# Kernel tuning notes

Measured on AMD Instinct MI355X. Metric: run time of the kernel, lower is better.

## Reference

```python
import jax, jax.numpy as jnp
import numpy as np

B, L, D1, D2 = 4, 2048, 1024, 1024

def setup_inputs() -> dict:
    key = jax.random.key(0)
    k1, k2, k3, k4, k5, k6 = jax.random.split(key, 6)
    s1 = 1.0 / np.sqrt(D1)
    s2 = 1.0 / np.sqrt(D2)
    return {
        "features_1": jax.random.normal(k1, (B, L, D1), dtype=jnp.float32),
        "features_2": jax.random.normal(k2, (B, L, D2), dtype=jnp.float32),
        # nn.Linear(d1, d2): W1 [d2, d1], b1 [d2]
        "W1": jax.random.uniform(k3, (D2, D1), jnp.float32, -s1, s1),
        "b1": jax.random.uniform(k4, (D2,), jnp.float32, -s1, s1),
        # nn.Linear(d2, d1): W2 [d1, d2], b2 [d1]
        "W2": jax.random.uniform(k5, (D1, D2), jnp.float32, -s2, s2),
        "b2": jax.random.uniform(k6, (D1,), jnp.float32, -s2, s2),
    }

def reference(features_1, features_2, W1, b1, W2, b2):
    # transformed_features_1: [B, L, D2]
    t1 = jnp.einsum('bld,ed->ble', features_1, W1) + b1
    # unscaled similarity: [B, L, L]
    sim = jnp.einsum('ble,bme->blm', t1, features_2)
    attn = jax.nn.softmax(sim, axis=-1)  # both softmaxes are identical
    attended_1 = jnp.einsum('blm,bme->ble', attn, features_2)  # [B, L, D2]
    attended_2 = jnp.einsum('blm,bme->ble', attn, t1)          # [B, L, D2]
    attended_2 = jnp.einsum('ble,de->bld', attended_2, W2) + b2  # [B, L, D1]
    return attended_1, attended_2
```

## Files before the change

kernel.cpp:

```cpp
#include <hip/hip_runtime.h>
#include <stdint.h>

#define BB 4
#define LL 2048
#define DD 1024

typedef __attribute__((ext_vector_type(4))) float f32x4;
typedef __attribute__((ext_vector_type(8))) _Float16 f16x8;
typedef __attribute__((ext_vector_type(4))) unsigned short u16x4;
typedef __attribute__((ext_vector_type(8))) unsigned short u16x8;
typedef unsigned short u16;

__device__ __forceinline__ u16 f2h(float x){
  return __builtin_bit_cast(u16, (_Float16)x);
}

__device__ __forceinline__ void gload16(const u16* g, u16* l){
  __builtin_amdgcn_global_load_lds((const __attribute__((address_space(1))) unsigned*)g,
                                   (__attribute__((address_space(3))) unsigned*)l,
                                   16, 0, 0);
}

__device__ __forceinline__ int xcd_swz(int bx, int nwg){
  return (bx & 7) * (nwg >> 3) + (bx >> 3);
}

__device__ __forceinline__ void stage_tile8(u16* lds, const u16* src, int ld, int wave, int lane){
  const int r0 = lane >> 3;
  const int cs = (((lane & 7) ^ r0) << 3);
  #pragma unroll
  for (int j = 0; j < 2; ++j){
    const int rb = wave*16 + j*8;
    gload16(src + (size_t)(rb + r0)*ld + cs, lds + rb*64);
  }
}

__device__ __forceinline__ f16x8 frag_ld(const u16* t, int row, int ko){
  return __builtin_bit_cast(f16x8,
    *reinterpret_cast<const f32x4*>(t + row*64 + (ko ^ ((row & 7) << 3))));
}

__global__ void cast3_k(const float* __restrict__ f1, u16* __restrict__ f1f,
                        const float* __restrict__ W1, u16* __restrict__ w1f,
                        const float* __restrict__ W2, u16* __restrict__ w2f){
  const int n1 = (BB*LL*DD)/4, nw = (DD*DD)/4;
  const int stride = gridDim.x * blockDim.x;
  for (int i = blockIdx.x*blockDim.x + threadIdx.x; i < n1 + 2*nw; i += stride){
    const float* s; u16* d; int k;
    if (i < n1){ s = f1; d = f1f; k = i; }
    else if (i < n1 + nw){ s = W1; d = w1f; k = i - n1; }
    else { s = W2; d = w2f; k = i - n1 - nw; }
    f32x4 v = reinterpret_cast<const f32x4*>(s)[k];
    u16x4 h;
    #pragma unroll
    for (int j = 0; j < 4; ++j) h[j] = f2h(v[j]);
    reinterpret_cast<u16x4*>(d)[k] = h;
  }
}

__global__ void castT_k(const float* __restrict__ f2, u16* __restrict__ f2f,
                        u16* __restrict__ f2T){
  __shared__ u16 t[32][33];
  const int b = blockIdx.z;
  const int d0 = blockIdx.x*32, l0 = blockIdx.y*32;
  const float* src = f2 + (size_t)b*LL*DD;
  u16* d1 = f2f + (size_t)b*LL*DD;
  u16* d2 = f2T + (size_t)b*DD*LL;
  const int x = threadIdx.x;
  for (int j = threadIdx.y; j < 32; j += 8){
    u16 h = f2h(src[(size_t)(l0+j)*DD + d0 + x]);
    d1[(size_t)(l0+j)*DD + d0 + x] = h;
    t[j][x] = h;
  }
  __syncthreads();
  for (int j = threadIdx.y; j < 32; j += 8)
    d2[(size_t)(d0+j)*LL + l0 + x] = t[x][j];
}

__global__ __launch_bounds__(512,2) void gemm8p_k(
    const u16* __restrict__ A_g, long long sAb, int lda,
    const u16* __restrict__ B_g, long long sBb, int ldb,
    float* __restrict__ C, long long sCb, int ldc, int NT){
  __shared__ __align__(16) u16 As[4][128*64];
  __shared__ __align__(16) u16 Bs[4][128*64];
  const int b = blockIdx.y;
  const int bx = xcd_swz(blockIdx.x, gridDim.x);
  const int bm = bx >> 3, bn = bx & 7;
  const int tid = threadIdx.x, wave = tid>>6, lane = tid&63;
  const int wm = wave & 1, wn = wave >> 1;
  const int r0 = lane >> 3, cs = (((lane&7) ^ r0) << 3);
  const int rb0 = wave*16;
  const u16* Ab = A_g + (size_t)b*sAb + (size_t)(bm*256)*lda;
  const u16* Bb = B_g + (size_t)b*sBb + (size_t)(bn*256)*ldb;

  f32x4 acc[2][2][4][2];
  #pragma unroll
  for (int i=0;i<2;i++)
    #pragma unroll
    for (int j=0;j<2;j++)
      #pragma unroll
      for (int m=0;m<4;m++)
        #pragma unroll
        for (int n=0;n<2;n++) acc[i][j][m][n] = (f32x4){0.f,0.f,0.f,0.f};

  auto stA = [&](int tt, int h){
    const u16* s = Ab + (size_t)(h*128 + rb0 + r0)*lda + (size_t)tt*64 + cs;
    u16* d = &As[((tt&1)<<1)+h][rb0*64];
    gload16(s, d);
    gload16(s + (size_t)8*lda, d + 8*64);
  };
  auto stB = [&](int tt, int h){
    const u16* s = Bb + (size_t)(h*128 + rb0 + r0)*ldb + (size_t)tt*64 + cs;
    u16* d = &Bs[((tt&1)<<1)+h][rb0*64];
    gload16(s, d);
    gload16(s + (size_t)8*ldb, d + 8*64);
  };

  stA(0,0); stB(0,0); stA(0,1); stB(0,1);
  stA(1,0); stB(1,0);
  asm volatile("s_waitcnt vmcnt(4)" ::: "memory");
  __builtin_amdgcn_s_barrier();

  for (int t = 0; t < NT; ++t){
    #pragma unroll
    for (int p = 0; p < 4; ++p){
      const u16* Ah = As[((t&1)<<1) + (p>>1)];
      const u16* Bh = Bs[((t&1)<<1) + (p&1)];
      f16x8 af[4][2], bf[2][2];
      #pragma unroll
      for (int mi=0;mi<4;mi++)
        #pragma unroll
        for (int ks=0;ks<2;ks++)
          af[mi][ks] = frag_ld(Ah, wm*64 + mi*16 + (lane&15), ks*32 + ((lane>>4)<<3));
      #pragma unroll
      for (int ni=0;ni<2;ni++)
        #pragma unroll
        for (int ks=0;ks<2;ks++)
          bf[ni][ks] = frag_ld(Bh, wn*32 + ni*16 + (lane&15), ks*32 + ((lane>>4)<<3));
      if (p == 0){ if (t+1 < NT) stA(t+1, 1); }
      else if (p == 1){ if (t+1 < NT) stB(t+1, 1); }
      else if (p == 2){ if (t+2 < NT) stA(t+2, 0); }
      else {
        if (t+2 < NT){ stB(t+2, 0); asm volatile("s_waitcnt vmcnt(4)" ::: "memory"); }
        else         {              asm volatile("s_waitcnt vmcnt(0)" ::: "memory"); }
      }
      __builtin_amdgcn_s_barrier();
      asm volatile("s_waitcnt lgkmcnt(0)" ::: "memory");
      __builtin_amdgcn_sched_barrier(0);
      __builtin_amdgcn_s_setprio(1);
      #pragma unroll
      for (int mi=0;mi<4;mi++)
        #pragma unroll
        for (int ni=0;ni<2;ni++)
          #pragma unroll
          for (int ks=0;ks<2;ks++)
            acc[p>>1][p&1][mi][ni] = __builtin_amdgcn_mfma_f32_16x16x32_f16(
                af[mi][ks], bf[ni][ks], acc[p>>1][p&1][mi][ni], 0,0,0);
      __builtin_amdgcn_s_setprio(0);
      __builtin_amdgcn_sched_barrier(0);
      __builtin_amdgcn_s_barrier();
    }
  }

  #pragma unroll
  for (int qm=0;qm<2;qm++)
    #pragma unroll
    for (int qn=0;qn<2;qn++)
      #pragma unroll
      for (int mi=0;mi<4;mi++)
        #pragma unroll
        for (int ni=0;ni<2;ni++){
          const int r = bm*256 + qm*128 + wm*64 + mi*16 + ((lane>>4)<<2);
          const int c = bn*256 + qn*128 + wn*32 + ni*16 + (lane&15);
          float* Cb = C + (size_t)b*sCb;
          #pragma unroll
          for (int j=0;j<4;j++)
            Cb[(size_t)(r+j)*ldc + c] = acc[qm][qn][mi][ni][j];
        }
}

__global__ __launch_bounds__(512,4) void gemm_t1_k(
    const u16* __restrict__ A_g, const u16* __restrict__ B_g,
    const float* __restrict__ bias, u16* __restrict__ Oh){
  __shared__ __align__(16) u16 As[128*64];
  __shared__ __align__(16) u16 Bs[128*64];
  const int bx = xcd_swz(blockIdx.x, gridDim.x);
  const int bm = bx >> 3, bn = bx & 7;
  const int tid = threadIdx.x, wave = tid>>6, lane = tid&63;
  const int wr = wave>>2, wc = wave&3;
  const u16* Ab = A_g + (size_t)(bm*128)*DD;
  const u16* Bb = B_g + (size_t)(bn*128)*DD;
  f32x4 acc[4][2];
  #pragma unroll
  for (int i=0;i<4;i++)
    #pragma unroll
    for (int j=0;j<2;j++) acc[i][j] = (f32x4){0.f,0.f,0.f,0.f};

  for (int k0 = 0; k0 < DD; k0 += 64){
    __syncthreads();
    stage_tile8(As, Ab + k0, DD, wave, lane);
    stage_tile8(Bs, Bb + k0, DD, wave, lane);
    __syncthreads();
    #pragma unroll
    for (int kk=0;kk<2;kk++){
      const int ko = kk*32 + ((lane>>4)<<3);
      f16x8 a[4], bb[2];
      #pragma unroll
      for (int mi=0;mi<4;mi++) a[mi]  = frag_ld(As, wr*64 + mi*16 + (lane&15), ko);
      #pragma unroll
      for (int ni=0;ni<2;ni++) bb[ni] = frag_ld(Bs, wc*32 + ni*16 + (lane&15), ko);
      #pragma unroll
      for (int mi=0;mi<4;mi++)
        #pragma unroll
        for (int ni=0;ni<2;ni++)
          acc[mi][ni] = __builtin_amdgcn_mfma_f32_16x16x32_f16(a[mi], bb[ni], acc[mi][ni], 0,0,0);
    }
  }
  #pragma unroll
  for (int mi=0;mi<4;mi++)
    #pragma unroll
    for (int ni=0;ni<2;ni++){
      const int r = bm*128 + wr*64 + mi*16 + ((lane>>4)<<2);
      const int c = bn*128 + wc*32 + ni*16 + (lane&15);
      const float bv = bias[c];
      #pragma unroll
      for (int j=0;j<4;j++)
        Oh[(size_t)(r+j)*DD + c] = f2h(acc[mi][ni][j] + bv);
    }
}

__global__ __launch_bounds__(256) void softmax_k(float* __restrict__ sim){
  const int row = blockIdx.x;
  float* p = sim + (size_t)row * LL;
  const int tid = threadIdx.x, wave = tid>>6, lane = tid&63;
  f32x4 x0 = reinterpret_cast<const f32x4*>(p)[tid];
  f32x4 x1 = reinterpret_cast<const f32x4*>(p)[tid + 256];
  float mx = fmaxf(fmaxf(fmaxf(x0[0],x0[1]), fmaxf(x0[2],x0[3])),
                   fmaxf(fmaxf(x1[0],x1[1]), fmaxf(x1[2],x1[3])));
  #pragma unroll
  for (int o = 32; o; o >>= 1) mx = fmaxf(mx, __shfl_xor(mx, o, 64));
  __shared__ float red[8];
  if (lane == 0) red[wave] = mx;
  __syncthreads();
  mx = fmaxf(fmaxf(red[0], red[1]), fmaxf(red[2], red[3]));
  float e0[4], e1[4], s = 0.f;
  #pragma unroll
  for (int j=0;j<4;j++){ e0[j] = __expf(x0[j]-mx); s += e0[j]; }
  #pragma unroll
  for (int j=0;j<4;j++){ e1[j] = __expf(x1[j]-mx); s += e1[j]; }
  #pragma unroll
  for (int o = 32; o; o >>= 1) s += __shfl_xor(s, o, 64);
  if (lane == 0) red[4+wave] = s;
  __syncthreads();
  s = (red[4]+red[5]) + (red[6]+red[7]);
  const float inv = 1.0f / s;
  u16* ob = reinterpret_cast<u16*>(p);
  u16x4 w0, w1;
  #pragma unroll
  for (int j=0;j<4;j++){ w0[j] = f2h(e0[j]*inv); w1[j] = f2h(e1[j]*inv); }
  reinterpret_cast<u16x4*>(ob)[tid]       = w0;
  reinterpret_cast<u16x4*>(ob)[tid + 256] = w1;
}

__global__ __launch_bounds__(512,4) void gemm_zt_k(const u16* __restrict__ t1f,
                                                   const u16* __restrict__ w2f,
                                                   u16* __restrict__ ZT){
  __shared__ __align__(16) u16 As[128*64];
  __shared__ __align__(16) u16 Bs[128*64];
  __shared__ u16 T[128*132];
  const int bx = xcd_swz(blockIdx.x, gridDim.x);
  const int bm = bx >> 3, bn = bx & 7;
  const int tid = threadIdx.x, wave = tid>>6, lane = tid&63;
  const int wr = wave>>2, wc = wave&3;
  const u16* Ab = t1f + (size_t)(bm*128)*DD;
  const u16* Bb = w2f + (size_t)(bn*128)*DD;
  f32x4 acc[4][2];
  #pragma unroll
  for (int i=0;i<4;i++)
    #pragma unroll
    for (int j=0;j<2;j++) acc[i][j] = (f32x4){0.f,0.f,0.f,0.f};

  for (int k0 = 0; k0 < DD; k0 += 64){
    __syncthreads();
    stage_tile8(As, Ab + k0, DD, wave, lane);
    stage_tile8(Bs, Bb + k0, DD, wave, lane);
    __syncthreads();
    #pragma unroll
    for (int kk=0;kk<2;kk++){
      const int ko = kk*32 + ((lane>>4)<<3);
      f16x8 a[4], bb[2];
      #pragma unroll
      for (int mi=0;mi<4;mi++) a[mi]  = frag_ld(As, wr*64 + mi*16 + (lane&15), ko);
      #pragma unroll
      for (int ni=0;ni<2;ni++) bb[ni] = frag_ld(Bs, wc*32 + ni*16 + (lane&15), ko);
      #pragma unroll
      for (int mi=0;mi<4;mi++)
        #pragma unroll
        for (int ni=0;ni<2;ni++)
          acc[mi][ni] = __builtin_amdgcn_mfma_f32_16x16x32_f16(a[mi], bb[ni], acc[mi][ni], 0,0,0);
    }
  }
  #pragma unroll
  for (int mi=0;mi<4;mi++)
    #pragma unroll
    for (int ni=0;ni<2;ni++){
      const int r = wr*64 + mi*16 + ((lane>>4)<<2);
      const int c = wc*32 + ni*16 + (lane&15);
      #pragma unroll
      for (int j=0;j<4;j++)
        T[(r+j)*132 + c] = f2h(acc[mi][ni][j]);
    }
  __syncthreads();
  const int b2i = bm >> 4;
  const int mb  = (bm*128) & 2047;
  const int d   = tid >> 2, m0 = (tid & 3) << 5;
  u16* dst = ZT + ((size_t)b2i*DD + bn*128 + d)*LL + mb + m0;
  #pragma unroll
  for (int g = 0; g < 4; ++g){
    u16x8 v;
    #pragma unroll
    for (int e = 0; e < 8; ++e) v[e] = T[(m0 + g*8 + e)*132 + d];
    *reinterpret_cast<u16x8*>(dst + g*8) = v;
  }
}

__global__ __launch_bounds__(512,4) void gemm_pv_k(const u16* __restrict__ attn,
                                                   const u16* __restrict__ f2T,
                                                   const u16* __restrict__ ZT,
                                                   float* __restrict__ out1,
                                                   float* __restrict__ out2,
                                                   const float* __restrict__ b2){
  __shared__ __align__(16) u16 As[128*64];
  __shared__ __align__(16) u16 Bs[128*64];
  const int b = blockIdx.y;
  const int bx = xcd_swz(blockIdx.x, gridDim.x);
  const int bm = bx >> 4, bn = bx & 15;
  const int tid = threadIdx.x, wave = tid>>6, lane = tid&63;
  const int wr = wave>>2, wc = wave&3;
  const u16* Ab = attn + (size_t)b*LL*4096 + (size_t)(bm*128)*4096;
  const u16* Bbase = (bn < 8) ? f2T : ZT;
  const int d0 = (bn & 7) * 128;
  const u16* Bb = Bbase + (size_t)b*DD*LL + (size_t)d0*LL;
  f32x4 acc[4][2];
  #pragma unroll
  for (int i=0;i<4;i++)
    #pragma unroll
    for (int j=0;j<2;j++) acc[i][j] = (f32x4){0.f,0.f,0.f,0.f};

  for (int k0 = 0; k0 < LL; k0 += 64){
    __syncthreads();
    stage_tile8(As, Ab + k0, 4096, wave, lane);
    stage_tile8(Bs, Bb + k0, LL, wave, lane);
    __syncthreads();
    #pragma unroll
    for (int kk=0;kk<2;kk++){
      const int ko = kk*32 + ((lane>>4)<<3);
      f16x8 a[4], bb[2];
      #pragma unroll
      for (int mi=0;mi<4;mi++) a[mi]  = frag_ld(As, wr*64 + mi*16 + (lane&15), ko);
      #pragma unroll
      for (int ni=0;ni<2;ni++) bb[ni] = frag_ld(Bs, wc*32 + ni*16 + (lane&15), ko);
      #pragma unroll
      for (int mi=0;mi<4;mi++)
        #pragma unroll
        for (int ni=0;ni<2;ni++)
          acc[mi][ni] = __builtin_amdgcn_mfma_f32_16x16x32_f16(a[mi], bb[ni], acc[mi][ni], 0,0,0);
    }
  }
  float* O = ((bn < 8) ? out1 : out2) + (size_t)b*LL*DD;
  const bool has_bias = (bn >= 8);
  #pragma unroll
  for (int mi=0;mi<4;mi++)
    #pragma unroll
    for (int ni=0;ni<2;ni++){
      const int r = bm*128 + wr*64 + mi*16 + ((lane>>4)<<2);
      const int c = d0 + wc*32 + ni*16 + (lane&15);
      const float bv = has_bias ? b2[c] : 0.f;
      #pragma unroll
      for (int j=0;j<4;j++)
        O[(size_t)(r+j)*DD + c] = acc[mi][ni][j] + bv;
    }
}

extern "C" void kernel_launch(void* const* d_in, const int* in_sizes, int n_in,
                              void* d_out, int out_size, void* d_ws, size_t ws_size,
                              hipStream_t stream) {
  const float* f1 = (const float*)d_in[0];
  const float* f2 = (const float*)d_in[1];
  const float* W1 = (const float*)d_in[2];
  const float* b1 = (const float*)d_in[3];
  const float* W2 = (const float*)d_in[4];
  const float* b2 = (const float*)d_in[5];
  float* out1 = (float*)d_out;
  float* out2 = out1 + (size_t)BB*LL*DD;

  char* ws = (char*)d_ws;
  u16* t1f = (u16*)(ws + 0);
  u16* ZT  = (u16*)(ws + 16777216);
  u16* f2f = (u16*)(ws + 33554432);
  u16* f2T = (u16*)(ws + 50331648);
  u16* w1f = (u16*)(ws + 67108864);
  u16* w2f = (u16*)(ws + 69206016);
  float* sim = (float*)(ws + 71303168);
  u16* f1f = (u16*)(ws + 71303168);

  castT_k<<<dim3(32, 64, BB), dim3(32, 8), 0, stream>>>(f2, f2f, f2T);
  cast3_k<<<4096, 256, 0, stream>>>(f1, f1f, W1, w1f, W2, w2f);
  gemm_t1_k<<<dim3(512, 1), 512, 0, stream>>>(f1f, w1f, b1, t1f);
  gemm8p_k<<<dim3(64, BB), 512, 0, stream>>>(t1f, (long long)LL*DD, DD,
                                             f2f, (long long)LL*DD, DD,
                                             sim, (long long)LL*LL, LL, 16);
  softmax_k<<<BB*LL, 256, 0, stream>>>(sim);
  gemm_zt_k<<<dim3(512, 1), 512, 0, stream>>>(t1f, w2f, ZT);
  gemm_pv_k<<<dim3(256, BB), 512, 0, stream>>>((const u16*)sim, f2T, ZT,
                                               out1, out2, b2);
}
```

Baseline: 209.7 us.

## Precompute W2·W1 to fuse Z with t1 and merge the two PV GEMMs

Uses the identity t1·W2ᵀ = f1·(W2W1)ᵀ + W2·b1. A small GEMM forms W12 = W2·W1, and a single kernel then computes t1 and Zᵀ together from one shared f1 tile. This removes the serial t1 → Z GEMM dependency and the extra A-tile reloads. The folded bias W2·b1 + b2 is added after attention, which is valid because softmax rows sum to one. The PV step now computes both outputs in one kernel that reads each attention tile once against two B tiles. In exchange it uses more LDS per block, launches fewer blocks, adds two small kernels, and changes fp16 rounding behaviour.

```diff
diff --git a/kernel.cpp b/kernel.cpp
--- a/kernel.cpp
+++ b/kernel.cpp
@@ -40,16 +40,14 @@
     *reinterpret_cast<const f32x4*>(t + row*64 + (ko ^ ((row & 7) << 3))));
 }
 
-__global__ void cast3_k(const float* __restrict__ f1, u16* __restrict__ f1f,
-                        const float* __restrict__ W1, u16* __restrict__ w1f,
+__global__ void cast2_k(const float* __restrict__ f1, u16* __restrict__ f1f,
                         const float* __restrict__ W2, u16* __restrict__ w2f){
   const int n1 = (BB*LL*DD)/4, nw = (DD*DD)/4;
   const int stride = gridDim.x * blockDim.x;
-  for (int i = blockIdx.x*blockDim.x + threadIdx.x; i < n1 + 2*nw; i += stride){
+  for (int i = blockIdx.x*blockDim.x + threadIdx.x; i < n1 + nw; i += stride){
     const float* s; u16* d; int k;
     if (i < n1){ s = f1; d = f1f; k = i; }
-    else if (i < n1 + nw){ s = W1; d = w1f; k = i - n1; }
-    else { s = W2; d = w2f; k = i - n1 - nw; }
+    else { s = W2; d = w2f; k = i - n1; }
     f32x4 v = reinterpret_cast<const f32x4*>(s)[k];
     u16x4 h;
     #pragma unroll
@@ -59,14 +57,18 @@
 }
 
 __global__ void castT_k(const float* __restrict__ f2, u16* __restrict__ f2f,
-                        u16* __restrict__ f2T){
+                        u16* __restrict__ f2T,
+                        const float* __restrict__ W1, u16* __restrict__ w1f,
+                        u16* __restrict__ w1T){
   __shared__ u16 t[32][33];
-  const int b = blockIdx.z;
+  const int z = blockIdx.z;
   const int d0 = blockIdx.x*32, l0 = blockIdx.y*32;
-  const float* src = f2 + (size_t)b*LL*DD;
-  u16* d1 = f2f + (size_t)b*LL*DD;
-  u16* d2 = f2T + (size_t)b*DD*LL;
+  const float* src; u16* d1; u16* d2; int nrow;
+  if (z < 4){ src = f2 + (size_t)z*LL*DD; d1 = f2f + (size_t)z*LL*DD; d2 = f2T + (size_t)z*DD*LL; nrow = LL; }
+  else      { src = W1; d1 = w1f; d2 = w1T; nrow = DD; }
+  if (l0 >= nrow) return;
   const int x = threadIdx.x;
+  const int ldT = (z < 4) ? LL : DD;
   for (int j = threadIdx.y; j < 32; j += 8){
     u16 h = f2h(src[(size_t)(l0+j)*DD + d0 + x]);
     d1[(size_t)(l0+j)*DD + d0 + x] = h;
@@ -74,7 +76,158 @@
   }
   __syncthreads();
   for (int j = threadIdx.y; j < 32; j += 8)
-    d2[(size_t)(d0+j)*LL + l0 + x] = t[x][j];
+    d2[(size_t)(d0+j)*ldT + l0 + x] = t[x][j];
+}
+
+__global__ __launch_bounds__(512) void bz2_k(const float* __restrict__ W2,
+                                             const float* __restrict__ b1,
+                                             const float* __restrict__ b2,
+                                             float* __restrict__ bz2){
+  const int wave = threadIdx.x >> 6, lane = threadIdx.x & 63;
+  const int d = blockIdx.x*8 + wave;
+  float s = 0.f;
+  #pragma unroll
+  for (int k = 0; k < 16; ++k){
+    const int e = lane + (k << 6);
+    s += W2[(size_t)d*DD + e] * b1[e];
+  }
+  #pragma unroll
+  for (int o = 32; o; o >>= 1) s += __shfl_xor(s, o, 64);
+  if (lane == 0) bz2[d] = b2[d] + s;
+}
+
+__global__ __launch_bounds__(512,4) void w12_k(const u16* __restrict__ A_g,
+                                               const u16* __restrict__ B_g,
+                                               u16* __restrict__ Oh){
+  __shared__ __align__(16) u16 As[128*64];
+  __shared__ __align__(16) u16 Bs[128*64];
+  const int bx = xcd_swz(blockIdx.x, gridDim.x);
+  const int bm = bx >> 3, bn = bx & 7;
+  const int tid = threadIdx.x, wave = tid>>6, lane = tid&63;
+  const int wr = wave>>2, wc = wave&3;
+  const u16* Ab = A_g + (size_t)(bm*128)*DD;
+  const u16* Bb = B_g + (size_t)(bn*128)*DD;
+  f32x4 acc[4][2];
+  #pragma unroll
+  for (int i=0;i<4;i++)
+    #pragma unroll
+    for (int j=0;j<2;j++) acc[i][j] = (f32x4){0.f,0.f,0.f,0.f};
+  for (int k0 = 0; k0 < DD; k0 += 64){
+    __syncthreads();
+    stage_tile8(As, Ab + k0, DD, wave, lane);
+    stage_tile8(Bs, Bb + k0, DD, wave, lane);
+    __syncthreads();
+    #pragma unroll
+    for (int kk=0;kk<2;kk++){
+      const int ko = kk*32 + ((lane>>4)<<3);
+      f16x8 a[4], bb[2];
+      #pragma unroll
+      for (int mi=0;mi<4;mi++) a[mi]  = frag_ld(As, wr*64 + mi*16 + (lane&15), ko);
+      #pragma unroll
+      for (int ni=0;ni<2;ni++) bb[ni] = frag_ld(Bs, wc*32 + ni*16 + (lane&15), ko);
+      #pragma unroll
+      for (int mi=0;mi<4;mi++)
+        #pragma unroll
+        for (int ni=0;ni<2;ni++)
+          acc[mi][ni] = __builtin_amdgcn_mfma_f32_16x16x32_f16(a[mi], bb[ni], acc[mi][ni], 0,0,0);
+    }
+  }
+  #pragma unroll
+  for (int mi=0;mi<4;mi++)
+    #pragma unroll
+    for (int ni=0;ni<2;ni++){
+      const int r = bm*128 + wr*64 + mi*16 + ((lane>>4)<<2);
+      const int c = bn*128 + wc*32 + ni*16 + (lane&15);
+      #pragma unroll
+      for (int j=0;j<4;j++)
+        Oh[(size_t)(r+j)*DD + c] = f2h(acc[mi][ni][j]);
+    }
+}
+
+__global__ __launch_bounds__(512,4) void t1z_k(const u16* __restrict__ f1f,
+                                               const u16* __restrict__ w1f,
+                                               const u16* __restrict__ w12f,
+                                               const float* __restrict__ b1,
+                                               u16* __restrict__ t1f,
+                                               u16* __restrict__ ZT){
+  __shared__ __align__(16) u16 SH[3*128*64];
+  u16* As  = SH;
+  u16* B1s = SH + 8192;
+  u16* B2s = SH + 16384;
+  const int bx = xcd_swz(blockIdx.x, gridDim.x);
+  const int bm = bx >> 3, bn = bx & 7;
+  const int tid = threadIdx.x, wave = tid>>6, lane = tid&63;
+  const int wr = wave>>2, wc = wave&3;
+  const u16* Ab  = f1f  + (size_t)(bm*128)*DD;
+  const u16* B1b = w1f  + (size_t)(bn*128)*DD;
+  const u16* B2b = w12f + (size_t)(bn*128)*DD;
+  f32x4 acc1[4][2], acc2[4][2];
+  #pragma unroll
+  for (int i=0;i<4;i++)
+    #pragma unroll
+    for (int j=0;j<2;j++){ acc1[i][j] = (f32x4){0.f,0.f,0.f,0.f}; acc2[i][j] = acc1[i][j]; }
+
+  for (int k0 = 0; k0 < DD; k0 += 64){
+    __syncthreads();
+    stage_tile8(As,  Ab  + k0, DD, wave, lane);
+    stage_tile8(B1s, B1b + k0, DD, wave, lane);
+    stage_tile8(B2s, B2b + k0, DD, wave, lane);
+    __syncthreads();
+    #pragma unroll
+    for (int kk=0;kk<2;kk++){
+      const int ko = kk*32 + ((lane>>4)<<3);
+      f16x8 a[4], b1v[2], b2v[2];
+      #pragma unroll
+      for (int mi=0;mi<4;mi++) a[mi]  = frag_ld(As, wr*64 + mi*16 + (lane&15), ko);
+      #pragma unroll
+      for (int ni=0;ni<2;ni++){
+        b1v[ni] = frag_ld(B1s, wc*32 + ni*16 + (lane&15), ko);
+        b2v[ni] = frag_ld(B2s, wc*32 + ni*16 + (lane&15), ko);
+      }
+      #pragma unroll
+      for (int mi=0;mi<4;mi++)
+        #pragma unroll
+        for (int ni=0;ni<2;ni++){
+          acc1[mi][ni] = __builtin_amdgcn_mfma_f32_16x16x32_f16(a[mi], b1v[ni], acc1[mi][ni], 0,0,0);
+          acc2[mi][ni] = __builtin_amdgcn_mfma_f32_16x16x32_f16(a[mi], b2v[ni], acc2[mi][ni], 0,0,0);
+        }
+    }
+  }
+  #pragma unroll
+  for (int mi=0;mi<4;mi++)
+    #pragma unroll
+    for (int ni=0;ni<2;ni++){
+      const int r = bm*128 + wr*64 + mi*16 + ((lane>>4)<<2);
+      const int c = bn*128 + wc*32 + ni*16 + (lane&15);
+      const float bv = b1[c];
+      #pragma unroll
+      for (int j=0;j<4;j++)
+        t1f[(size_t)(r+j)*DD + c] = f2h(acc1[mi][ni][j] + bv);
+    }
+  __syncthreads();
+  u16* T = SH;
+  #pragma unroll
+  for (int mi=0;mi<4;mi++)
+    #pragma unroll
+    for (int ni=0;ni<2;ni++){
+      const int r = wr*64 + mi*16 + ((lane>>4)<<2);
+      const int c = wc*32 + ni*16 + (lane&15);
+      #pragma unroll
+      for (int j=0;j<4;j++)
+        T[(r+j)*132 + c] = f2h(acc2[mi][ni][j]);
+    }
+  __syncthreads();
+  const int b2i = bm >> 4;
+  const int mb  = (bm*128) & 2047;
+  const int d   = tid >> 2, m0 = (tid & 3) << 5;
+  u16* dst = ZT + ((size_t)b2i*DD + bn*128 + d)*LL + mb + m0;
+  #pragma unroll
+  for (int g = 0; g < 4; ++g){
+    u16x8 v;
+    #pragma unroll
+    for (int e = 0; e < 8; ++e) v[e] = T[(m0 + g*8 + e)*132 + d];
+    *reinterpret_cast<u16x8*>(dst + g*8) = v;
+  }
 }
 
 __global__ __launch_bounds__(512,2) void gemm8p_k(
@@ -179,56 +332,6 @@
         }
 }
 
-__global__ __launch_bounds__(512,4) void gemm_t1_k(
-    const u16* __restrict__ A_g, const u16* __restrict__ B_g,
-    const float* __restrict__ bias, u16* __restrict__ Oh){
-  __shared__ __align__(16) u16 As[128*64];
-  __shared__ __align__(16) u16 Bs[128*64];
-  const int bx = xcd_swz(blockIdx.x, gridDim.x);
-  const int bm = bx >> 3, bn = bx & 7;
-  const int tid = threadIdx.x, wave = tid>>6, lane = tid&63;
-  const int wr = wave>>2, wc = wave&3;
-  const u16* Ab = A_g + (size_t)(bm*128)*DD;
-  const u16* Bb = B_g + (size_t)(bn*128)*DD;
-  f32x4 acc[4][2];
-  #pragma unroll
-  for (int i=0;i<4;i++)
-    #pragma unroll
-    for (int j=0;j<2;j++) acc[i][j] = (f32x4){0.f,0.f,0.f,0.f};
-
-  for (int k0 = 0; k0 < DD; k0 += 64){
-    __syncthreads();
-    stage_tile8(As, Ab + k0, DD, wave, lane);
-    stage_tile8(Bs, Bb + k0, DD, wave, lane);
-    __syncthreads();
-    #pragma unroll
-    for (int kk=0;kk<2;kk++){
-      const int ko = kk*32 + ((lane>>4)<<3);
-      f16x8 a[4], bb[2];
-      #pragma unroll
-      for (int mi=0;mi<4;mi++) a[mi]  = frag_ld(As, wr*64 + mi*16 + (lane&15), ko);
-      #pragma unroll
-      for (int ni=0;ni<2;ni++) bb[ni] = frag_ld(Bs, wc*32 + ni*16 + (lane&15), ko);
-      #pragma unroll
-      for (int mi=0;mi<4;mi++)
-        #pragma unroll
-        for (int ni=0;ni<2;ni++)
-          acc[mi][ni] = __builtin_amdgcn_mfma_f32_16x16x32_f16(a[mi], bb[ni], acc[mi][ni], 0,0,0);
-    }
-  }
-  #pragma unroll
-  for (int mi=0;mi<4;mi++)
-    #pragma unroll
-    for (int ni=0;ni<2;ni++){
-      const int r = bm*128 + wr*64 + mi*16 + ((lane>>4)<<2);
-      const int c = bn*128 + wc*32 + ni*16 + (lane&15);
-      const float bv = bias[c];
-      #pragma unroll
-      for (int j=0;j<4;j++)
-        Oh[(size_t)(r+j)*DD + c] = f2h(acc[mi][ni][j] + bv);
-    }
-}
-
 __global__ __launch_bounds__(256) void softmax_k(float* __restrict__ sim){
   const int row = blockIdx.x;
   float* p = sim + (size_t)row * LL;
@@ -262,123 +365,69 @@
   reinterpret_cast<u16x4*>(ob)[tid + 256] = w1;
 }
 
-__global__ __launch_bounds__(512,4) void gemm_zt_k(const u16* __restrict__ t1f,
-                                                   const u16* __restrict__ w2f,
-                                                   u16* __restrict__ ZT){
+__global__ __launch_bounds__(512,4) void pv2_k(const u16* __restrict__ attn,
+                                               const u16* __restrict__ f2T,
+                                               const u16* __restrict__ ZT,
+                                               float* __restrict__ out1,
+                                               float* __restrict__ out2,
+                                               const float* __restrict__ bz2){
   __shared__ __align__(16) u16 As[128*64];
-  __shared__ __align__(16) u16 Bs[128*64];
-  __shared__ u16 T[128*132];
+  __shared__ __align__(16) u16 B1s[128*64];
+  __shared__ __align__(16) u16 B2s[128*64];
+  const int b = blockIdx.y;
   const int bx = xcd_swz(blockIdx.x, gridDim.x);
-  const int bm = bx >> 3, bn = bx & 7;
+  const int bm = bx >> 3, dn = bx & 7;
   const int tid = threadIdx.x, wave = tid>>6, lane = tid&63;
   const int wr = wave>>2, wc = wave&3;
-  const u16* Ab = t1f + (size_t)(bm*128)*DD;
-  const u16* Bb = w2f + (size_t)(bn*128)*DD;
-  f32x4 acc[4][2];
+  const u16* Ab  = attn + (size_t)b*LL*4096 + (size_t)(bm*128)*4096;
+  const u16* B1b = f2T + (size_t)b*DD*LL + (size_t)(dn*128)*LL;
+  const u16* B2b = ZT  + (size_t)b*DD*LL + (size_t)(dn*128)*LL;
+  f32x4 acc1[4][2], acc2[4][2];
   #pragma unroll
   for (int i=0;i<4;i++)
     #pragma unroll
-    for (int j=0;j<2;j++) acc[i][j] = (f32x4){0.f,0.f,0.f,0.f};
-
-  for (int k0 = 0; k0 < DD; k0 += 64){
-    __syncthreads();
-    stage_tile8(As, Ab + k0, DD, wave, lane);
-    stage_tile8(Bs, Bb + k0, DD, wave, lane);
+    for (int j=0;j<2;j++){ acc1[i][j] = (f32x4){0.f,0.f,0.f,0.f}; acc2[i][j] = acc1[i][j]; }
+
+  for (int k0 = 0; k0 < LL; k0 += 64){
+    __syncthreads();
+    stage_tile8(As,  Ab  + k0, 4096, wave, lane);
+    stage_tile8(B1s, B1b + k0, LL, wave, lane);
+    stage_tile8(B2s, B2b + k0, LL, wave, lane);
     __syncthreads();
     #pragma unroll
     for (int kk=0;kk<2;kk++){
       const int ko = kk*32 + ((lane>>4)<<3);
-      f16x8 a[4], bb[2];
+      f16x8 a[4], b1v[2], b2v[2];
       #pragma unroll
       for (int mi=0;mi<4;mi++) a[mi]  = frag_ld(As, wr*64 + mi*16 + (lane&15), ko);
       #pragma unroll
-      for (int ni=0;ni<2;ni++) bb[ni] = frag_ld(Bs, wc*32 + ni*16 + (lane&15), ko);
-      #pragma unroll
-      for (int mi=0;mi<4;mi++)
-        #pragma unroll
-        for (int ni=0;ni<2;ni++)
-          acc[mi][ni] = __builtin_amdgcn_mfma_f32_16x16x32_f16(a[mi], bb[ni], acc[mi][ni], 0,0,0);
-    }
-  }
-  #pragma unroll
-  for (int mi=0;mi<4;mi++)
-    #pragma unroll
-    for (int ni=0;ni<2;ni++){
-      const int r = wr*64 + mi*16 + ((lane>>4)<<2);
-      const int c = wc*32 + ni*16 + (lane&15);
-      #pragma unroll
-      for (int j=0;j<4;j++)
-        T[(r+j)*132 + c] = f2h(acc[mi][ni][j]);
-    }
-  __syncthreads();
-  const int b2i = bm >> 4;
-  const int mb  = (bm*128) & 2047;
-  const int d   = tid >> 2, m0 = (tid & 3) << 5;
-  u16* dst = ZT + ((size_t)b2i*DD + bn*128 + d)*LL + mb + m0;
-  #pragma unroll
-  for (int g = 0; g < 4; ++g){
-    u16x8 v;
-    #pragma unroll
-    for (int e = 0; e < 8; ++e) v[e] = T[(m0 + g*8 + e)*132 + d];
-    *reinterpret_cast<u16x8*>(dst + g*8) = v;
-  }
-}
-
-__global__ __launch_bounds__(512,4) void gemm_pv_k(const u16* __restrict__ attn,
-                                                   const u16* __restrict__ f2T,
-                                                   const u16* __restrict__ ZT,
-                                                   float* __restrict__ out1,
-                                                   float* __restrict__ out2,
-                                                   const float* __restrict__ b2){
-  __shared__ __align__(16) u16 As[128*64];
-  __shared__ __align__(16) u16 Bs[128*64];
-  const int b = blockIdx.y;
-  const int bx = xcd_swz(blockIdx.x, gridDim.x);
-  const int bm = bx >> 4, bn = bx & 15;
-  const int tid = threadIdx.x, wave = tid>>6, lane = tid&63;
-  const int wr = wave>>2, wc = wave&3;
-  const u16* Ab = attn + (size_t)b*LL*4096 + (size_t)(bm*128)*4096;
-  const u16* Bbase = (bn < 8) ? f2T : ZT;
-  const int d0 = (bn & 7) * 128;
-  const u16* Bb = Bbase + (size_t)b*DD*LL + (size_t)d0*LL;
-  f32x4 acc[4][2];
-  #pragma unroll
-  for (int i=0;i<4;i++)
-    #pragma unroll
-    for (int j=0;j<2;j++) acc[i][j] = (f32x4){0.f,0.f,0.f,0.f};
-
-  for (int k0 = 0; k0 < LL; k0 += 64){
-    __syncthreads();
-    stage_tile8(As, Ab + k0, 4096, wave, lane);
-    stage_tile8(Bs, Bb + k0, LL, wave, lane);
-    __syncthreads();
-    #pragma unroll
-    for (int kk=0;kk<2;kk++){
-      const int ko = kk*32 + ((lane>>4)<<3);
-      f16x8 a[4], bb[2];
-      #pragma unroll
-      for (int mi=0;mi<4;mi++) a[mi]  = frag_ld(As, wr*64 + mi*16 + (lane&15), ko);
-      #pragma unroll
-      for (int ni=0;ni<2;ni++) bb[ni] = frag_ld(Bs, wc*32 + ni*16 + (lane&15), ko);
-      #pragma unroll
-      for (int mi=0;mi<4;mi++)
-        #pragma unroll
-        for (int ni=0;ni<2;ni++)
-          acc[mi][ni] = __builtin_amdgcn_mfma_f32_16x16x32_f16(a[mi], bb[ni], acc[mi][ni], 0,0,0);
-    }
-  }
-  float* O = ((bn < 8) ? out1 : out2) + (size_t)b*LL*DD;
-  const bool has_bias = (bn >= 8);
+      for (int ni=0;ni<2;ni++){
+        b1v[ni] = frag_ld(B1s, wc*32 + ni*16 + (lane&15), ko);
+        b2v[ni] = frag_ld(B2s, wc*32 + ni*16 + (lane&15), ko);
+      }
+      #pragma unroll
+      for (int mi=0;mi<4;mi++)
+        #pragma unroll
+        for (int ni=0;ni<2;ni++){
+          acc1[mi][ni] = __builtin_amdgcn_mfma_f32_16x16x32_f16(a[mi], b1v[ni], acc1[mi][ni], 0,0,0);
+          acc2[mi][ni] = __builtin_amdgcn_mfma_f32_16x16x32_f16(a[mi], b2v[ni], acc2[mi][ni], 0,0,0);
+        }
+    }
+  }
+  float* O1 = out1 + (size_t)b*LL*DD;
+  float* O2 = out2 + (size_t)b*LL*DD;
   #pragma unroll
   for (int mi=0;mi<4;mi++)
     #pragma unroll
     for (int ni=0;ni<2;ni++){
       const int r = bm*128 + wr*64 + mi*16 + ((lane>>4)<<2);
-      const int c = d0 + wc*32 + ni*16 + (lane&15);
-      const float bv = has_bias ? b2[c] : 0.f;
-      #pragma unroll
-      for (int j=0;j<4;j++)
-        O[(size_t)(r+j)*DD + c] = acc[mi][ni][j] + bv;
+      const int c = dn*128 + wc*32 + ni*16 + (lane&15);
+      const float bv = bz2[c];
+      #pragma unroll
+      for (int j=0;j<4;j++){
+        O1[(size_t)(r+j)*DD + c] = acc1[mi][ni][j];
+        O2[(size_t)(r+j)*DD + c] = acc2[mi][ni][j] + bv;
+      }
     }
 }
 
@@ -399,19 +448,23 @@
   u16* ZT  = (u16*)(ws + 16777216);
   u16* f2f = (u16*)(ws + 33554432);
   u16* f2T = (u16*)(ws + 50331648);
-  u16* w1f = (u16*)(ws + 67108864);
-  u16* w2f = (u16*)(ws + 69206016);
-  float* sim = (float*)(ws + 71303168);
-  u16* f1f = (u16*)(ws + 71303168);
-
-  castT_k<<<dim3(32, 64, BB), dim3(32, 8), 0, stream>>>(f2, f2f, f2T);
-  cast3_k<<<4096, 256, 0, stream>>>(f1, f1f, W1, w1f, W2, w2f);
-  gemm_t1_k<<<dim3(512, 1), 512, 0, stream>>>(f1f, w1f, b1, t1f);
+  float* sim = (float*)(ws + 67108864);
+  u16* f1f  = (u16*)(ws + 67108864);
+  u16* w1T  = (u16*)(ws + 67108864 + 16777216);
+  u16* w12f = (u16*)(ws + 67108864 + 18874368);
+  u16* w2f  = (u16*)(ws + 67108864 + 20971520);
+  u16* w1f  = (u16*)(ws + 67108864 + 23068672);
+  float* bz2 = (float*)(ws + 134217728);
+
+  castT_k<<<dim3(32, 64, 5), dim3(32, 8), 0, stream>>>(f2, f2f, f2T, W1, w1f, w1T);
+  cast2_k<<<4096, 256, 0, stream>>>(f1, f1f, W2, w2f);
+  bz2_k<<<128, 512, 0, stream>>>(W2, b1, b2, bz2);
+  w12_k<<<64, 512, 0, stream>>>(w2f, w1T, w12f);
+  t1z_k<<<512, 512, 0, stream>>>(f1f, w1f, w12f, b1, t1f, ZT);
   gemm8p_k<<<dim3(64, BB), 512, 0, stream>>>(t1f, (long long)LL*DD, DD,
                                              f2f, (long long)LL*DD, DD,
                                              sim, (long long)LL*LL, LL, 16);
   softmax_k<<<BB*LL, 256, 0, stream>>>(sim);
-  gemm_zt_k<<<dim3(512, 1), 512, 0, stream>>>(t1f, w2f, ZT);
-  gemm_pv_k<<<dim3(256, BB), 512, 0, stream>>>((const u16*)sim, f2T, ZT,
-                                               out1, out2, b2);
-}
+  pv2_k<<<dim3(128, BB), 512, 0, stream>>>((const u16*)sim, f2T, ZT,
+                                           out1, out2, bz2);
+}
```

Result: slower. 287.5 us (+37.1%).

## Replace sim and PV GEMMs with shared 256x128 fat-tile templated kernel

Applied to the files above, without the earlier changes.

Replaces the software-pipelined 256x256 similarity GEMM and the 128x128 attention-times-values GEMM with one templated kernel. It uses 256x128 tiles with 4 waves, each computing a 128x64 sub-tile, which gives more register-level reuse per LDS fragment load. The new kernel is single-buffered with a sync before and after each K step, so it gives up the earlier kernel's load/compute overlap and fine-grained barriers. The larger accumulator also raises register pressure, which may limit occupancy.

```diff
diff --git a/kernel.cpp b/kernel.cpp
--- a/kernel.cpp
+++ b/kernel.cpp
@@ -31,6 +31,25 @@
   #pragma unroll
   for (int j = 0; j < 2; ++j){
     const int rb = wave*16 + j*8;
+    gload16(src + (size_t)(rb + r0)*ld + cs, lds + rb*64);
+  }
+}
+
+__device__ __forceinline__ void stage_fatA(u16* lds, const u16* src, int ld, int wave, int lane){
+  const int r0 = lane >> 3;
+  const int cs = (((lane & 7) ^ r0) << 3);
+  #pragma unroll
+  for (int j = 0; j < 8; ++j){
+    const int rb = wave*64 + j*8;
+    gload16(src + (size_t)(rb + r0)*ld + cs, lds + rb*64);
+  }
+}
+__device__ __forceinline__ void stage_fatB(u16* lds, const u16* src, int ld, int wave, int lane){
+  const int r0 = lane >> 3;
+  const int cs = (((lane & 7) ^ r0) << 3);
+  #pragma unroll
+  for (int j = 0; j < 4; ++j){
+    const int rb = wave*32 + j*8;
     gload16(src + (size_t)(rb + r0)*ld + cs, lds + rb*64);
   }
 }
@@ -77,108 +96,6 @@
     d2[(size_t)(d0+j)*LL + l0 + x] = t[x][j];
 }
 
-__global__ __launch_bounds__(512,2) void gemm8p_k(
-    const u16* __restrict__ A_g, long long sAb, int lda,
-    const u16* __restrict__ B_g, long long sBb, int ldb,
-    float* __restrict__ C, long long sCb, int ldc, int NT){
-  __shared__ __align__(16) u16 As[4][128*64];
-  __shared__ __align__(16) u16 Bs[4][128*64];
-  const int b = blockIdx.y;
-  const int bx = xcd_swz(blockIdx.x, gridDim.x);
-  const int bm = bx >> 3, bn = bx & 7;
-  const int tid = threadIdx.x, wave = tid>>6, lane = tid&63;
-  const int wm = wave & 1, wn = wave >> 1;
-  const int r0 = lane >> 3, cs = (((lane&7) ^ r0) << 3);
-  const int rb0 = wave*16;
-  const u16* Ab = A_g + (size_t)b*sAb + (size_t)(bm*256)*lda;
-  const u16* Bb = B_g + (size_t)b*sBb + (size_t)(bn*256)*ldb;
-
-  f32x4 acc[2][2][4][2];
-  #pragma unroll
-  for (int i=0;i<2;i++)
-    #pragma unroll
-    for (int j=0;j<2;j++)
-      #pragma unroll
-      for (int m=0;m<4;m++)
-        #pragma unroll
-        for (int n=0;n<2;n++) acc[i][j][m][n] = (f32x4){0.f,0.f,0.f,0.f};
-
-  auto stA = [&](int tt, int h){
-    const u16* s = Ab + (size_t)(h*128 + rb0 + r0)*lda + (size_t)tt*64 + cs;
-    u16* d = &As[((tt&1)<<1)+h][rb0*64];
-    gload16(s, d);
-    gload16(s + (size_t)8*lda, d + 8*64);
-  };
-  auto stB = [&](int tt, int h){
-    const u16* s = Bb + (size_t)(h*128 + rb0 + r0)*ldb + (size_t)tt*64 + cs;
-    u16* d = &Bs[((tt&1)<<1)+h][rb0*64];
-    gload16(s, d);
-    gload16(s + (size_t)8*ldb, d + 8*64);
-  };
-
-  stA(0,0); stB(0,0); stA(0,1); stB(0,1);
-  stA(1,0); stB(1,0);
-  asm volatile("s_waitcnt vmcnt(4)" ::: "memory");
-  __builtin_amdgcn_s_barrier();
-
-  for (int t = 0; t < NT; ++t){
-    #pragma unroll
-    for (int p = 0; p < 4; ++p){
-      const u16* Ah = As[((t&1)<<1) + (p>>1)];
-      const u16* Bh = Bs[((t&1)<<1) + (p&1)];
-      f16x8 af[4][2], bf[2][2];
-      #pragma unroll
-      for (int mi=0;mi<4;mi++)
-        #pragma unroll
-        for (int ks=0;ks<2;ks++)
-          af[mi][ks] = frag_ld(Ah, wm*64 + mi*16 + (lane&15), ks*32 + ((lane>>4)<<3));
-      #pragma unroll
-      for (int ni=0;ni<2;ni++)
-        #pragma unroll
-        for (int ks=0;ks<2;ks++)
-          bf[ni][ks] = frag_ld(Bh, wn*32 + ni*16 + (lane&15), ks*32 + ((lane>>4)<<3));
-      if (p == 0){ if (t+1 < NT) stA(t+1, 1); }
-      else if (p == 1){ if (t+1 < NT) stB(t+1, 1); }
-      else if (p == 2){ if (t+2 < NT) stA(t+2, 0); }
-      else {
-        if (t+2 < NT){ stB(t+2, 0); asm volatile("s_waitcnt vmcnt(4)" ::: "memory"); }
-        else         {              asm volatile("s_waitcnt vmcnt(0)" ::: "memory"); }
-      }
-      __builtin_amdgcn_s_barrier();
-      asm volatile("s_waitcnt lgkmcnt(0)" ::: "memory");
-      __builtin_amdgcn_sched_barrier(0);
-      __builtin_amdgcn_s_setprio(1);
-      #pragma unroll
-      for (int mi=0;mi<4;mi++)
-        #pragma unroll
-        for (int ni=0;ni<2;ni++)
-          #pragma unroll
-          for (int ks=0;ks<2;ks++)
-            acc[p>>1][p&1][mi][ni] = __builtin_amdgcn_mfma_f32_16x16x32_f16(
-                af[mi][ks], bf[ni][ks], acc[p>>1][p&1][mi][ni], 0,0,0);
-      __builtin_amdgcn_s_setprio(0);
-      __builtin_amdgcn_sched_barrier(0);
-      __builtin_amdgcn_s_barrier();
-    }
-  }
-
-  #pragma unroll
-  for (int qm=0;qm<2;qm++)
-    #pragma unroll
-    for (int qn=0;qn<2;qn++)
-      #pragma unroll
-      for (int mi=0;mi<4;mi++)
-        #pragma unroll
-        for (int ni=0;ni<2;ni++){
-          const int r = bm*256 + qm*128 + wm*64 + mi*16 + ((lane>>4)<<2);
-          const int c = bn*256 + qn*128 + wn*32 + ni*16 + (lane&15);
-          float* Cb = C + (size_t)b*sCb;
-          #pragma unroll
-          for (int j=0;j<4;j++)
-            Cb[(size_t)(r+j)*ldc + c] = acc[qm][qn][mi][ni][j];
-        }
-}
-
 __global__ __launch_bounds__(512,4) void gemm_t1_k(
     const u16* __restrict__ A_g, const u16* __restrict__ B_g,
     const float* __restrict__ bias, u16* __restrict__ Oh){
@@ -227,39 +144,6 @@
       for (int j=0;j<4;j++)
         Oh[(size_t)(r+j)*DD + c] = f2h(acc[mi][ni][j] + bv);
     }
-}
-
-__global__ __launch_bounds__(256) void softmax_k(float* __restrict__ sim){
-  const int row = blockIdx.x;
-  float* p = sim + (size_t)row * LL;
-  const int tid = threadIdx.x, wave = tid>>6, lane = tid&63;
-  f32x4 x0 = reinterpret_cast<const f32x4*>(p)[tid];
-  f32x4 x1 = reinterpret_cast<const f32x4*>(p)[tid + 256];
-  float mx = fmaxf(fmaxf(fmaxf(x0[0],x0[1]), fmaxf(x0[2],x0[3])),
-                   fmaxf(fmaxf(x1[0],x1[1]), fmaxf(x1[2],x1[3])));
-  #pragma unroll
-  for (int o = 32; o; o >>= 1) mx = fmaxf(mx, __shfl_xor(mx, o, 64));
-  __shared__ float red[8];
-  if (lane == 0) red[wave] = mx;
-  __syncthreads();
-  mx = fmaxf(fmaxf(red[0], red[1]), fmaxf(red[2], red[3]));
-  float e0[4], e1[4], s = 0.f;
-  #pragma unroll
-  for (int j=0;j<4;j++){ e0[j] = __expf(x0[j]-mx); s += e0[j]; }
-  #pragma unroll
-  for (int j=0;j<4;j++){ e1[j] = __expf(x1[j]-mx); s += e1[j]; }
-  #pragma unroll
-  for (int o = 32; o; o >>= 1) s += __shfl_xor(s, o, 64);
-  if (lane == 0) red[4+wave] = s;
-  __syncthreads();
-  s = (red[4]+red[5]) + (red[6]+red[7]);
-  const float inv = 1.0f / s;
-  u16* ob = reinterpret_cast<u16*>(p);
-  u16x4 w0, w1;
-  #pragma unroll
-  for (int j=0;j<4;j++){ w0[j] = f2h(e0[j]*inv); w1[j] = f2h(e1[j]*inv); }
-  reinterpret_cast<u16x4*>(ob)[tid]       = w0;
-  reinterpret_cast<u16x4*>(ob)[tid + 256] = w1;
 }
 
 __global__ __launch_bounds__(512,4) void gemm_zt_k(const u16* __restrict__ t1f,
@@ -324,62 +208,113 @@
   }
 }
 
-__global__ __launch_bounds__(512,4) void gemm_pv_k(const u16* __restrict__ attn,
-                                                   const u16* __restrict__ f2T,
-                                                   const u16* __restrict__ ZT,
-                                                   float* __restrict__ out1,
-                                                   float* __restrict__ out2,
-                                                   const float* __restrict__ b2){
-  __shared__ __align__(16) u16 As[128*64];
+__global__ __launch_bounds__(256) void softmax_k(float* __restrict__ sim){
+  const int row = blockIdx.x;
+  float* p = sim + (size_t)row * LL;
+  const int tid = threadIdx.x, wave = tid>>6, lane = tid&63;
+  f32x4 x0 = reinterpret_cast<const f32x4*>(p)[tid];
+  f32x4 x1 = reinterpret_cast<const f32x4*>(p)[tid + 256];
+  float mx = fmaxf(fmaxf(fmaxf(x0[0],x0[1]), fmaxf(x0[2],x0[3])),
+                   fmaxf(fmaxf(x1[0],x1[1]), fmaxf(x1[2],x1[3])));
+  #pragma unroll
+  for (int o = 32; o; o >>= 1) mx = fmaxf(mx, __shfl_xor(mx, o, 64));
+  __shared__ float red[8];
+  if (lane == 0) red[wave] = mx;
+  __syncthreads();
+  mx = fmaxf(fmaxf(red[0], red[1]), fmaxf(red[2], red[3]));
+  float e0[4], e1[4], s = 0.f;
+  #pragma unroll
+  for (int j=0;j<4;j++){ e0[j] = __expf(x0[j]-mx); s += e0[j]; }
+  #pragma unroll
+  for (int j=0;j<4;j++){ e1[j] = __expf(x1[j]-mx); s += e1[j]; }
+  #pragma unroll
+  for (int o = 32; o; o >>= 1) s += __shfl_xor(s, o, 64);
+  if (lane == 0) red[4+wave] = s;
+  __syncthreads();
+  s = (red[4]+red[5]) + (red[6]+red[7]);
+  const float inv = 1.0f / s;
+  u16* ob = reinterpret_cast<u16*>(p);
+  u16x4 w0, w1;
+  #pragma unroll
+  for (int j=0;j<4;j++){ w0[j] = f2h(e0[j]*inv); w1[j] = f2h(e1[j]*inv); }
+  reinterpret_cast<u16x4*>(ob)[tid]       = w0;
+  reinterpret_cast<u16x4*>(ob)[tid + 256] = w1;
+}
+
+template<int EPI>
+__global__ __launch_bounds__(256,3) void gemmf_k(
+    const u16* __restrict__ A_g, long long sAb, int lda,
+    const u16* __restrict__ B0_g, const u16* __restrict__ B1_g, long long sBb, int ldb,
+    float* __restrict__ C0, float* __restrict__ C1, long long sCb, int ldc,
+    const float* __restrict__ bias, int K, int tn_sh){
+  __shared__ __align__(16) u16 As[256*64];
   __shared__ __align__(16) u16 Bs[128*64];
   const int b = blockIdx.y;
   const int bx = xcd_swz(blockIdx.x, gridDim.x);
-  const int bm = bx >> 4, bn = bx & 15;
+  const int bm = bx >> tn_sh, bn = bx & ((1 << tn_sh) - 1);
   const int tid = threadIdx.x, wave = tid>>6, lane = tid&63;
-  const int wr = wave>>2, wc = wave&3;
-  const u16* Ab = attn + (size_t)b*LL*4096 + (size_t)(bm*128)*4096;
-  const u16* Bbase = (bn < 8) ? f2T : ZT;
-  const int d0 = (bn & 7) * 128;
-  const u16* Bb = Bbase + (size_t)b*DD*LL + (size_t)d0*LL;
-  f32x4 acc[4][2];
-  #pragma unroll
-  for (int i=0;i<4;i++)
-    #pragma unroll
-    for (int j=0;j<2;j++) acc[i][j] = (f32x4){0.f,0.f,0.f,0.f};
-
-  for (int k0 = 0; k0 < LL; k0 += 64){
-    __syncthreads();
-    stage_tile8(As, Ab + k0, 4096, wave, lane);
-    stage_tile8(Bs, Bb + k0, LL, wave, lane);
+  const int wm = wave >> 1, wn = wave & 1;
+  const u16* Ab = A_g + (size_t)b*sAb + (size_t)(bm*256)*lda;
+  const u16* Bb;
+  if (EPI == 0){
+    Bb = B0_g + (size_t)b*sBb + (size_t)(bn*128)*ldb;
+  } else {
+    Bb = ((bn < 8) ? B0_g : B1_g) + (size_t)b*sBb + (size_t)((bn&7)*128)*ldb;
+  }
+  f32x4 acc[8][4];
+  #pragma unroll
+  for (int i=0;i<8;i++)
+    #pragma unroll
+    for (int j=0;j<4;j++) acc[i][j] = (f32x4){0.f,0.f,0.f,0.f};
+
+  for (int k0 = 0; k0 < K; k0 += 64){
+    __syncthreads();
+    stage_fatA(As, Ab + k0, lda, wave, lane);
+    stage_fatB(Bs, Bb + k0, ldb, wave, lane);
     __syncthreads();
     #pragma unroll
     for (int kk=0;kk<2;kk++){
       const int ko = kk*32 + ((lane>>4)<<3);
-      f16x8 a[4], bb[2];
-      #pragma unroll
-      for (int mi=0;mi<4;mi++) a[mi]  = frag_ld(As, wr*64 + mi*16 + (lane&15), ko);
-      #pragma unroll
-      for (int ni=0;ni<2;ni++) bb[ni] = frag_ld(Bs, wc*32 + ni*16 + (lane&15), ko);
-      #pragma unroll
-      for (int mi=0;mi<4;mi++)
-        #pragma unroll
-        for (int ni=0;ni<2;ni++)
-          acc[mi][ni] = __builtin_amdgcn_mfma_f32_16x16x32_f16(a[mi], bb[ni], acc[mi][ni], 0,0,0);
-    }
-  }
-  float* O = ((bn < 8) ? out1 : out2) + (size_t)b*LL*DD;
-  const bool has_bias = (bn >= 8);
-  #pragma unroll
-  for (int mi=0;mi<4;mi++)
-    #pragma unroll
-    for (int ni=0;ni<2;ni++){
-      const int r = bm*128 + wr*64 + mi*16 + ((lane>>4)<<2);
-      const int c = d0 + wc*32 + ni*16 + (lane&15);
-      const float bv = has_bias ? b2[c] : 0.f;
-      #pragma unroll
-      for (int j=0;j<4;j++)
-        O[(size_t)(r+j)*DD + c] = acc[mi][ni][j] + bv;
-    }
+      f16x8 af[8], bf[4];
+      #pragma unroll
+      for (int mi=0;mi<8;mi++) af[mi] = frag_ld(As, wm*128 + mi*16 + (lane&15), ko);
+      #pragma unroll
+      for (int ni=0;ni<4;ni++) bf[ni] = frag_ld(Bs, wn*64 + ni*16 + (lane&15), ko);
+      #pragma unroll
+      for (int mi=0;mi<8;mi++)
+        #pragma unroll
+        for (int ni=0;ni<4;ni++)
+          acc[mi][ni] = __builtin_amdgcn_mfma_f32_16x16x32_f16(af[mi], bf[ni], acc[mi][ni], 0,0,0);
+    }
+  }
+
+  if (EPI == 0){
+    float* Cb = C0 + (size_t)b*sCb;
+    #pragma unroll
+    for (int mi=0;mi<8;mi++)
+      #pragma unroll
+      for (int ni=0;ni<4;ni++){
+        const int r = bm*256 + wm*128 + mi*16 + ((lane>>4)<<2);
+        const int c = bn*128 + wn*64 + ni*16 + (lane&15);
+        #pragma unroll
+        for (int j=0;j<4;j++)
+          Cb[(size_t)(r+j)*ldc + c] = acc[mi][ni][j];
+      }
+  } else {
+    float* O = ((bn < 8) ? C0 : C1) + (size_t)b*sCb;
+    const bool has_bias = (bn >= 8);
+    #pragma unroll
+    for (int mi=0;mi<8;mi++)
+      #pragma unroll
+      for (int ni=0;ni<4;ni++){
+        const int r = bm*256 + wm*128 + mi*16 + ((lane>>4)<<2);
+        const int c = (bn&7)*128 + wn*64 + ni*16 + (lane&15);
+        const float bv = has_bias ? bias[c] : 0.f;
+        #pragma unroll
+        for (int j=0;j<4;j++)
+          O[(size_t)(r+j)*ldc + c] = acc[mi][ni][j] + bv;
+      }
+  }
 }
 
 extern "C" void kernel_launch(void* const* d_in, const int* in_sizes, int n_in,
@@ -407,11 +342,14 @@
   castT_k<<<dim3(32, 64, BB), dim3(32, 8), 0, stream>>>(f2, f2f, f2T);
   cast3_k<<<4096, 256, 0, stream>>>(f1, f1f, W1, w1f, W2, w2f);
   gemm_t1_k<<<dim3(512, 1), 512, 0, stream>>>(f1f, w1f, b1, t1f);
-  gemm8p_k<<<dim3(64, BB), 512, 0, stream>>>(t1f, (long long)LL*DD, DD,
-                                             f2f, (long long)LL*DD, DD,
-                                             sim, (long long)LL*LL, LL, 16);
+  gemmf_k<0><<<dim3(128, BB), 256, 0, stream>>>(t1f, (long long)LL*DD, DD,
+                                                f2f, nullptr, (long long)LL*DD, DD,
+                                                sim, nullptr, (long long)LL*LL, LL,
+                                                nullptr, DD, 4);
   softmax_k<<<BB*LL, 256, 0, stream>>>(sim);
   gemm_zt_k<<<dim3(512, 1), 512, 0, stream>>>(t1f, w2f, ZT);
-  gemm_pv_k<<<dim3(256, BB), 512, 0, stream>>>((const u16*)sim, f2T, ZT,
-                                               out1, out2, b2);
-}
+  gemmf_k<1><<<dim3(128, BB), 256, 0, stream>>>((const u16*)sim, (long long)LL*4096, 4096,
+                                                f2T, ZT, (long long)DD*LL, LL,
+                                                out1, out2, (long long)LL*DD, DD,
+                                                b2, LL, 4);
+}
```

After: 395.3 us. 1.88x slower.
